# Kernel optimization log

Hardware: AMD Instinct MI355X
Metric: run time of the kernel (lower is better)

Reference implementation:

```python
import jax, jax.numpy as jnp
import numpy as np
import math

HEAD_DIM = 128
N_HEADS = 32
HIDDEN = 4096
ROPE_THETA = 10000.0
NEG = -100000.0


def _rope_cos_sin(pos):
    # pos: [B, L] int -> cos, sin: [B, L, HEAD_DIM]
    inv_freq = 1.0 / (ROPE_THETA ** (jnp.arange(0, HEAD_DIM, 2, dtype=jnp.float32) / HEAD_DIM))
    freqs = pos.astype(jnp.float32)[..., None] * inv_freq  # [B, L, HEAD_DIM//2]
    emb = jnp.concatenate([freqs, freqs], axis=-1)
    return jnp.cos(emb), jnp.sin(emb)


def _rotate_half(x):
    x1, x2 = x[..., : HEAD_DIM // 2], x[..., HEAD_DIM // 2 :]
    return jnp.concatenate([-x2, x1], axis=-1)


def _apply_rope(h, cos, sin):
    # h: [B, H, L, D], cos/sin: [B, L, D] -> unsqueeze head dim
    return h * cos[:, None] + _rotate_half(h) * sin[:, None]


def setup_inputs() -> dict:
    key = jax.random.key(0)
    ks = jax.random.split(key, 8)
    B, Q, K = 2, 1024, 2048
    inp = {
        "hidden_states": jax.random.normal(ks[0], (B, Q, HIDDEN), jnp.float32),
        "key_value_states": jax.random.normal(ks[1], (B, K, HIDDEN), jnp.float32),
        "Wq": jax.random.normal(ks[2], (HIDDEN, HIDDEN), jnp.float32) * 0.02,
        "Wk": jax.random.normal(ks[3], (HIDDEN, HIDDEN), jnp.float32) * 0.02,
        "Wv": jax.random.normal(ks[4], (HIDDEN, HIDDEN), jnp.float32) * 0.02,
        "Wo": jax.random.normal(ks[5], (HIDDEN, HIDDEN), jnp.float32) * 0.02,
        "position_ids": jnp.arange(B * Q, dtype=jnp.int32).reshape(B, Q),
        "text_position_ids": jnp.arange(B * K, dtype=jnp.int32).reshape(B, K),
        "simul_mask_idx": jnp.sort(jax.random.randint(ks[6], (B, Q), 0, K, jnp.int32), axis=-1),
        "window_size": jax.random.randint(ks[7], (B, Q), 0, 512, jnp.int32),
    }
    return inp


def reference(hidden_states, key_value_states, Wq, Wk, Wv, Wo,
              position_ids, text_position_ids, simul_mask_idx, window_size):
    B, Qlen, _ = hidden_states.shape
    Klen = key_value_states.shape[1]

    q = jnp.einsum('bqh,hd->bqd', hidden_states, Wq.T).reshape(B, Qlen, N_HEADS, HEAD_DIM).transpose(0, 2, 1, 3)
    k = jnp.einsum('bkh,hd->bkd', key_value_states, Wk.T).reshape(B, Klen, N_HEADS, HEAD_DIM).transpose(0, 2, 1, 3)
    v = jnp.einsum('bkh,hd->bkd', key_value_states, Wv.T).reshape(B, Klen, N_HEADS, HEAD_DIM).transpose(0, 2, 1, 3)

    cos, sin = _rope_cos_sin(position_ids)
    q = _apply_rope(q, cos, sin)
    t_cos, t_sin = _rope_cos_sin(text_position_ids)
    k = _apply_rope(k, t_cos, t_sin)

    scores = jnp.einsum('bhqd,bhkd->bhqk', q, k) / math.sqrt(HEAD_DIM)

    # simul windowed mask: key j visible for query i iff clamp(idx-w,0) <= j < idx
    idx = simul_mask_idx[:, None, :, None]          # [B,1,Q,1]
    w = window_size[:, None, :, None]               # [B,1,Q,1]
    tmp = jnp.arange(Klen, dtype=jnp.int32)         # [K]
    mask = (jnp.clip(idx - w, 0) <= tmp) & (tmp < idx)  # [B,1,Q,K]
    scores = jnp.where(mask, scores, NEG)

    probs = jax.nn.softmax(scores.astype(jnp.float32), axis=-1).astype(q.dtype)
    attn = jnp.einsum('bhqk,bhkd->bhqd', probs, v)
    attn = attn.transpose(0, 2, 1, 3).reshape(B, Qlen, HIDDEN)
    out = jnp.einsum('bqh,hd->bqd', attn, Wo.T)
    return out
```

## Files before the change

kernel.cpp:

```cpp
#include <hip/hip_runtime.h>
#include <stdint.h>

#define BATCH 2
#define QLEN 1024
#define KLEN 2048
#define NH 32
#define HD 128
#define HID 4096

typedef short bf16x8 __attribute__((ext_vector_type(8)));
typedef float f32x4 __attribute__((ext_vector_type(4)));
typedef unsigned short u16;

typedef const __attribute__((address_space(1))) void gvoid;
typedef __attribute__((address_space(3))) void lvoid;

__device__ __forceinline__ u16 f2bf(float f) {
  union { float f; uint32_t u; } x; x.f = f;
  uint32_t r = x.u + 0x7fffu + ((x.u >> 16) & 1u);
  return (u16)(r >> 16);
}
__device__ __forceinline__ float bf2f(u16 h) {
  union { uint32_t u; float f; } x; x.u = ((uint32_t)h) << 16;
  return x.f;
}
__device__ __forceinline__ f32x4 mfma16(bf16x8 a, bf16x8 b, f32x4 c) {
  return __builtin_amdgcn_mfma_f32_16x16x32_bf16(a, b, c, 0, 0, 0);
}
__device__ __forceinline__ void glds16(const u16* src, char* dst) {
  __builtin_amdgcn_global_load_lds((gvoid*)src, (lvoid*)dst, 16, 0, 0);
}

__global__ __launch_bounds__(256) void cvt_kernel(const float* __restrict__ in,
                                                  u16* __restrict__ out, int n) {
  int i = (blockIdx.x * 256 + threadIdx.x) * 8;
  if (i >= n) return;
  const float4* p = (const float4*)(in + i);
  float4 a = p[0], b = p[1];
  union { u16 h[8]; bf16x8 v; } u;
  u.h[0] = f2bf(a.x); u.h[1] = f2bf(a.y); u.h[2] = f2bf(a.z); u.h[3] = f2bf(a.w);
  u.h[4] = f2bf(b.x); u.h[5] = f2bf(b.y); u.h[6] = f2bf(b.z); u.h[7] = f2bf(b.w);
  *(bf16x8*)(out + i) = u.v;
}

#define RD_A(CB, ks, mf) (*(const bf16x8*)(lds + (CB) + (ks) * 16384 + (mf) * 1024 + rA))
#define RD_B(CB, ks, nf) (*(const bf16x8*)(lds + 65536 + (CB) + (ks) * 16384 + (nf) * 1024 + rB))

#define TILE256(CB, NB, K0N)                                                     \
  {                                                                              \
    bf16x8 af[4], bfr[4], af2[4];                                                \
    _Pragma("unroll") for (int x = 0; x < 4; x++) af[x] = RD_A(CB, 0, x);        \
    _Pragma("unroll") for (int x = 0; x < 4; x++) bfr[x] = RD_B(CB, 0, x);       \
    glds16(As0 + (K0N), dA + (NB));                                              \
    glds16(As1 + (K0N), dA + (NB) + 8192);                                       \
    __builtin_amdgcn_s_barrier();                                                \
    asm volatile("s_waitcnt lgkmcnt(0)" ::: "memory");                           \
    __builtin_amdgcn_sched_barrier(0);                                           \
    __builtin_amdgcn_s_setprio(1);                                               \
    _Pragma("unroll") for (int mf = 0; mf < 4; mf++)                             \
      _Pragma("unroll") for (int nf = 0; nf < 4; nf++)                           \
        acc[mf][nf] = mfma16(af[mf], bfr[nf], acc[mf][nf]);                      \
    __builtin_amdgcn_s_setprio(0);                                               \
    __builtin_amdgcn_s_barrier();                                                \
    _Pragma("unroll") for (int x = 0; x < 4; x++) af2[x] = RD_A(CB, 0, 4 + x);   \
    glds16(Bs0 + (K0N), dB + (NB));                                              \
    glds16(Bs1 + (K0N), dB + (NB) + 8192);                                       \
    asm volatile("s_waitcnt vmcnt(4)" ::: "memory");                             \
    __builtin_amdgcn_s_barrier();                                                \
    asm volatile("s_waitcnt lgkmcnt(0)" ::: "memory");                           \
    __builtin_amdgcn_sched_barrier(0);                                           \
    __builtin_amdgcn_s_setprio(1);                                               \
    _Pragma("unroll") for (int mf = 0; mf < 4; mf++)                             \
      _Pragma("unroll") for (int nf = 0; nf < 4; nf++)                           \
        acc[4 + mf][nf] = mfma16(af2[mf], bfr[nf], acc[4 + mf][nf]);             \
    __builtin_amdgcn_s_setprio(0);                                               \
    __builtin_amdgcn_s_barrier();                                                \
    _Pragma("unroll") for (int x = 0; x < 4; x++) af[x] = RD_A(CB, 1, x);        \
    _Pragma("unroll") for (int x = 0; x < 4; x++) bfr[x] = RD_B(CB, 1, x);       \
    glds16(As0 + (K0N) + 32, dA + (NB) + 16384);                                 \
    glds16(As1 + (K0N) + 32, dA + (NB) + 16384 + 8192);                          \
    __builtin_amdgcn_s_barrier();                                                \
    asm volatile("s_waitcnt lgkmcnt(0)" ::: "memory");                           \
    __builtin_amdgcn_sched_barrier(0);                                           \
    __builtin_amdgcn_s_setprio(1);                                               \
    _Pragma("unroll") for (int mf = 0; mf < 4; mf++)                             \
      _Pragma("unroll") for (int nf = 0; nf < 4; nf++)                           \
        acc[mf][nf] = mfma16(af[mf], bfr[nf], acc[mf][nf]);                      \
    __builtin_amdgcn_s_setprio(0);                                               \
    __builtin_amdgcn_s_barrier();                                                \
    _Pragma("unroll") for (int x = 0; x < 4; x++) af2[x] = RD_A(CB, 1, 4 + x);   \
    glds16(Bs0 + (K0N) + 32, dB + (NB) + 16384);                                 \
    glds16(Bs1 + (K0N) + 32, dB + (NB) + 16384 + 8192);                          \
    asm volatile("s_waitcnt vmcnt(4)" ::: "memory");                             \
    __builtin_amdgcn_s_barrier();                                                \
    asm volatile("s_waitcnt lgkmcnt(0)" ::: "memory");                           \
    __builtin_amdgcn_sched_barrier(0);                                           \
    __builtin_amdgcn_s_setprio(1);                                               \
    _Pragma("unroll") for (int mf = 0; mf < 4; mf++)                             \
      _Pragma("unroll") for (int nf = 0; nf < 4; nf++)                           \
        acc[4 + mf][nf] = mfma16(af2[mf], bfr[nf], acc[4 + mf][nf]);             \
    __builtin_amdgcn_s_setprio(0);                                               \
    __builtin_amdgcn_s_barrier();                                                \
  }

template <int EPI>
__global__ __launch_bounds__(512, 2) void gemm256(const u16* __restrict__ A,
                                                  const u16* __restrict__ Bw,
                                                  void* __restrict__ Cout,
                                                  int M, int N, int K) {
  (void)M;
  __shared__ alignas(16) char lds[131072];
  const int tid = threadIdx.x;
  const int lane = tid & 63, wv = tid >> 6;
  const int wvm = wv >> 2, wvn = wv & 3;
  const int g = lane >> 4, l16 = lane & 15;
  const int m0 = blockIdx.y * 256, n0 = blockIdx.x * 256;

  const int srow = tid >> 2;
  const int sg = (tid & 3) ^ ((srow >> 1) & 3);
  const u16* As0 = A + (size_t)(m0 + srow) * K + sg * 8;
  const u16* As1 = A + (size_t)(m0 + 128 + srow) * K + sg * 8;
  const u16* Bs0 = Bw + (size_t)(n0 + srow) * K + sg * 8;
  const u16* Bs1 = Bw + (size_t)(n0 + 128 + srow) * K + sg * 8;
  char* dA = lds + tid * 16;
  char* dB = lds + 65536 + tid * 16;

  const int rsw = (g ^ ((l16 >> 1) & 3)) << 4;
  const int rA = (wvm * 128 + l16) * 64 + rsw;
  const int rB = (wvn * 64 + l16) * 64 + rsw;

  f32x4 acc[8][4];
#pragma unroll
  for (int mf = 0; mf < 8; mf++)
#pragma unroll
    for (int nf = 0; nf < 4; nf++) acc[mf][nf] = (f32x4){0.f, 0.f, 0.f, 0.f};

  glds16(As0, dA);
  glds16(As1, dA + 8192);
  glds16(Bs0, dB);
  glds16(Bs1, dB + 8192);
  glds16(As0 + 32, dA + 16384);
  glds16(As1 + 32, dA + 16384 + 8192);
  glds16(Bs0 + 32, dB + 16384);
  glds16(Bs1 + 32, dB + 16384 + 8192);
  asm volatile("s_waitcnt vmcnt(4)" ::: "memory");
  __builtin_amdgcn_s_barrier();

  const int NT = K >> 6;
  for (int t = 0; t < NT; t += 2) {
    const int kA = (t + 1) * 64;
    TILE256(0, 32768, kA)
    const int kB = (((t + 2) < NT) ? (t + 2) : 0) * 64;
    TILE256(32768, 0, kB)
  }

  if (EPI == 2) {
    u16* C = (u16*)Cout;
#pragma unroll
    for (int mf = 0; mf < 8; mf++) {
      int rowb = m0 + wvm * 128 + mf * 16 + g * 4;
#pragma unroll
      for (int nf = 0; nf < 4; nf++) {
        int col = n0 + wvn * 64 + nf * 16 + l16;
#pragma unroll
        for (int j = 0; j < 4; j++)
          C[(size_t)(rowb + j) * N + col] = f2bf(acc[mf][nf][j]);
      }
    }
  } else {
    u16* C = (u16*)Cout;
#pragma unroll
    for (int mf = 0; mf < 8; mf++) {
      int rowb = m0 + wvm * 128 + mf * 16 + g * 4;
      int bb = rowb >> 11, tt = rowb & 2047;
#pragma unroll
      for (int nf = 0; nf < 4; nf++) {
        int col = n0 + wvn * 64 + nf * 16 + l16;
        uint64_t pk = (uint64_t)f2bf(acc[mf][nf][0]) |
                      ((uint64_t)f2bf(acc[mf][nf][1]) << 16) |
                      ((uint64_t)f2bf(acc[mf][nf][2]) << 32) |
                      ((uint64_t)f2bf(acc[mf][nf][3]) << 48);
        *(uint64_t*)(C + ((size_t)(bb * 4096 + col)) * 2048 + tt) = pk;
      }
    }
  }
}

#define RD_AT(CB, ks, mf) (*(const bf16x8*)(lds + (CB) + (ks) * 16384 + (mf) * 1024 + rA))
#define RD_BT(CB, ks, nf) (*(const bf16x8*)(lds + 65536 + (CB) + (ks) * 8192 + (nf) * 1024 + rB))

#define TILE256T(CB, CBB, NB, NBB, K0N)                                          \
  {                                                                              \
    bf16x8 af[4], bfr[4];                                                        \
    _Pragma("unroll") for (int x = 0; x < 4; x++) af[x] = RD_AT(CB, 0, x);       \
    _Pragma("unroll") for (int x = 0; x < 4; x++) bfr[x] = RD_BT(CBB, 0, x);     \
    glds16(AsT0 + (K0N), dAT + (NB));                                            \
    glds16(AsT1 + (K0N), dAT + (NB) + 8192);                                     \
    glds16(BsT0 + (K0N), dBT + (NBB));                                           \
    asm volatile("s_waitcnt vmcnt(3)" ::: "memory");                             \
    __builtin_amdgcn_s_barrier();                                                \
    asm volatile("s_waitcnt lgkmcnt(0)" ::: "memory");                           \
    __builtin_amdgcn_sched_barrier(0);                                           \
    __builtin_amdgcn_s_setprio(1);                                               \
    _Pragma("unroll") for (int mf = 0; mf < 4; mf++)                             \
      _Pragma("unroll") for (int nf = 0; nf < 4; nf++)                           \
        acc[mf][nf] = mfma16(af[mf], bfr[nf], acc[mf][nf]);                      \
    __builtin_amdgcn_s_setprio(0);                                               \
    __builtin_amdgcn_s_barrier();                                                \
    _Pragma("unroll") for (int x = 0; x < 4; x++) af[x] = RD_AT(CB, 1, x);       \
    _Pragma("unroll") for (int x = 0; x < 4; x++) bfr[x] = RD_BT(CBB, 1, x);     \
    glds16(AsT0 + (K0N) + 32, dAT + (NB) + 16384);                               \
    glds16(AsT1 + (K0N) + 32, dAT + (NB) + 16384 + 8192);                        \
    glds16(BsT0 + (K0N) + 32, dBT + (NBB) + 8192);                               \
    asm volatile("s_waitcnt vmcnt(3)" ::: "memory");                             \
    __builtin_amdgcn_s_barrier();                                                \
    asm volatile("s_waitcnt lgkmcnt(0)" ::: "memory");                           \
    __builtin_amdgcn_sched_barrier(0);                                           \
    __builtin_amdgcn_s_setprio(1);                                               \
    _Pragma("unroll") for (int mf = 0; mf < 4; mf++)                             \
      _Pragma("unroll") for (int nf = 0; nf < 4; nf++)                           \
        acc[mf][nf] = mfma16(af[mf], bfr[nf], acc[mf][nf]);                      \
    __builtin_amdgcn_s_setprio(0);                                               \
    __builtin_amdgcn_s_barrier();                                                \
  }

template <int EPI>
__global__ __launch_bounds__(512, 2) void gemm256T(const u16* __restrict__ W,
                                                   const u16* __restrict__ Act,
                                                   void* __restrict__ Cout,
                                                   int K) {
  __shared__ alignas(16) char lds[98304];
  const int tid = threadIdx.x;
  const int lane = tid & 63, wv = tid >> 6;
  const int wvm = wv >> 1, wvn = wv & 1;
  const int g = lane >> 4, l16 = lane & 15;
  const int m0 = blockIdx.y * 256;
  const int n0 = blockIdx.x * 128;

  const int srow = tid >> 2;
  const int sg = (tid & 3) ^ ((srow >> 1) & 3);
  const u16* AsT0 = W + (size_t)(m0 + srow) * K + sg * 8;
  const u16* AsT1 = W + (size_t)(m0 + 128 + srow) * K + sg * 8;
  const u16* BsT0 = Act + (size_t)(n0 + srow) * K + sg * 8;
  char* dAT = lds + tid * 16;
  char* dBT = lds + 65536 + tid * 16;

  const int rsw = (g ^ ((l16 >> 1) & 3)) << 4;
  const int rA = (wvm * 64 + l16) * 64 + rsw;
  const int rB = (wvn * 64 + l16) * 64 + rsw;

  f32x4 acc[4][4];
#pragma unroll
  for (int mf = 0; mf < 4; mf++)
#pragma unroll
    for (int nf = 0; nf < 4; nf++) acc[mf][nf] = (f32x4){0.f, 0.f, 0.f, 0.f};

  glds16(AsT0, dAT);
  glds16(AsT1, dAT + 8192);
  glds16(BsT0, dBT);
  glds16(AsT0 + 32, dAT + 16384);
  glds16(AsT1 + 32, dAT + 16384 + 8192);
  glds16(BsT0 + 32, dBT + 8192);
  asm volatile("s_waitcnt vmcnt(3)" ::: "memory");
  __builtin_amdgcn_s_barrier();

  const int NT = K >> 6;
  for (int t = 0; t < NT; t += 2) {
    const int kA = (t + 1) * 64;
    TILE256T(0, 0, 32768, 16384, kA)
    const int kB = (((t + 2) < NT) ? (t + 2) : 0) * 64;
    TILE256T(32768, 16384, 0, 0, kB)
  }

  if (EPI == 0) {
    float* C = (float*)Cout;
#pragma unroll
    for (int mf = 0; mf < 4; mf++) {
      int frow = m0 + wvm * 64 + mf * 16 + g * 4;
#pragma unroll
      for (int nf = 0; nf < 4; nf++) {
        int col = n0 + wvn * 64 + nf * 16 + l16;
        float4 v = {acc[mf][nf][0], acc[mf][nf][1], acc[mf][nf][2], acc[mf][nf][3]};
        *(float4*)(C + (size_t)col * HID + frow) = v;
      }
    }
  } else {
    u16* C = (u16*)Cout;
#pragma unroll
    for (int mf = 0; mf < 4; mf++) {
      int frow = m0 + wvm * 64 + mf * 16 + g * 4;
#pragma unroll
      for (int nf = 0; nf < 4; nf++) {
        int col = n0 + wvn * 64 + nf * 16 + l16;
        uint64_t pk = (uint64_t)f2bf(acc[mf][nf][0]) |
                      ((uint64_t)f2bf(acc[mf][nf][1]) << 16) |
                      ((uint64_t)f2bf(acc[mf][nf][2]) << 32) |
                      ((uint64_t)f2bf(acc[mf][nf][3]) << 48);
        *(uint64_t*)(C + (size_t)col * HID + frow) = pk;
      }
    }
  }
}

__global__ __launch_bounds__(256) void rope_kernel(const u16* __restrict__ x,
                                                   const int* __restrict__ pos,
                                                   u16* __restrict__ out,
                                                   int rowsPerB) {
  int row = blockIdx.x;
  int b = row / rowsPerB, r = row - b * rowsPerB;
  float p = (float)pos[row];
  int t = threadIdx.x;
  int h = t >> 3, i0 = (t & 7) * 8;
  const u16* xr = x + (size_t)row * HID + h * HD;
  bf16x8 lov = *(const bf16x8*)(xr + i0);
  bf16x8 hiv = *(const bf16x8*)(xr + 64 + i0);
  union { u16 h[8]; bf16x8 v; } olo, ohi;
#pragma unroll
  for (int j = 0; j < 8; j++) {
    float lo = bf2f((u16)lov[j]);
    float hi = bf2f((u16)hiv[j]);
    float f = exp2f(-(float)(i0 + j) * (13.287712379549449f / 64.0f));
    float ang = p * f;
    float s, c;
    sincosf(ang, &s, &c);
    olo.h[j] = f2bf(lo * c - hi * s);
    ohi.h[j] = f2bf(hi * c + lo * s);
  }
  u16* ob = out + ((size_t)((b * NH + h) * rowsPerB) + r) * HD;
  *(bf16x8*)(ob + i0) = olo.v;
  *(bf16x8*)(ob + 64 + i0) = ohi.v;
}

__global__ __launch_bounds__(256) void vmean_kernel(const u16* __restrict__ vt,
                                                    float* __restrict__ vm) {
  int row = blockIdx.x * 4 + (threadIdx.x >> 6);
  int lane = threadIdx.x & 63;
  const u16* p = vt + (size_t)row * KLEN;
  float s = 0.f;
#pragma unroll
  for (int it = 0; it < 4; it++) {
    bf16x8 v = *(const bf16x8*)(p + it * 512 + lane * 8);
#pragma unroll
    for (int j = 0; j < 8; j++) s += bf2f((u16)v[j]);
  }
  for (int off = 32; off; off >>= 1) s += __shfl_xor(s, off);
  if (lane == 0) vm[row] = s * (1.0f / (float)KLEN);
}

__global__ __launch_bounds__(256, 2) void attn_kernel(
    const u16* __restrict__ qb, const u16* __restrict__ kb,
    const u16* __restrict__ vt, const float* __restrict__ vm,
    const int* __restrict__ idxA, const int* __restrict__ wA,
    u16* __restrict__ aout) {
  __shared__ u16 Ks[32][136];
  __shared__ u16 Vs[128][40];
  __shared__ u16 Ps[4][16][40];
  __shared__ int sS[64], sE[64], sRange[2];

  const int tid = threadIdx.x, lane = tid & 63, wv = tid >> 6;
  const int g = lane >> 4, l16 = lane & 15;
  const int blk = blockIdx.x;
  const int qt = blk & 15, bh = blk >> 4, b = bh >> 5, h = bh & 31;
  const int q0 = qt * 64;
  const float SCALE = 0.08838834764831845f;

  if (tid < 64) {
    int e = idxA[b * QLEN + q0 + tid];
    int w = wA[b * QLEN + q0 + tid];
    int s = e - w;
    if (s < 0) s = 0;
    sS[tid] = s;
    sE[tid] = e;
  }
  __syncthreads();
  if (wv == 0) {
    int s_ = sS[lane], e_ = sE[lane];
    int mn = (e_ > s_) ? s_ : 0x7fffffff;
    int mx = (e_ > s_) ? e_ : 0;
    for (int off = 32; off; off >>= 1) {
      mn = min(mn, __shfl_xor(mn, off));
      mx = max(mx, __shfl_xor(mx, off));
    }
    if (lane == 0) { sRange[0] = mn; sRange[1] = mx; }
  }
  __syncthreads();
  const int klo = sRange[0], khi = sRange[1];

  int rs[4], re[4];
#pragma unroll
  for (int r = 0; r < 4; r++) {
    rs[r] = sS[wv * 16 + g * 4 + r];
    re[r] = sE[wv * 16 + g * 4 + r];
  }

  bf16x8 qf[4];
  {
    const u16* qp = qb + ((size_t)(bh * QLEN + q0 + wv * 16 + l16)) * HD + g * 8;
#pragma unroll
    for (int s4 = 0; s4 < 4; s4++) qf[s4] = *(const bf16x8*)(qp + s4 * 32);
  }

  f32x4 acc[8];
#pragma unroll
  for (int db = 0; db < 8; db++) acc[db] = (f32x4){0.f, 0.f, 0.f, 0.f};
  float mrow[4] = {-1e30f, -1e30f, -1e30f, -1e30f};
  float lsum[4] = {0.f, 0.f, 0.f, 0.f};

  if (klo < khi) {
    for (int t0 = (klo & ~31); t0 < khi; t0 += 32) {
      {
        int idx = tid * 8;
        int kr = idx >> 7, kc = idx & 127;
        *(bf16x8*)(&Ks[kr][kc]) =
            *(const bf16x8*)(kb + ((size_t)(bh * KLEN + t0 + kr)) * HD + kc);
        int kr2 = kr + 16;
        *(bf16x8*)(&Ks[kr2][kc]) =
            *(const bf16x8*)(kb + ((size_t)(bh * KLEN + t0 + kr2)) * HD + kc);
        int vr = idx >> 5, vc = idx & 31;
        *(bf16x8*)(&Vs[vr][vc]) =
            *(const bf16x8*)(vt + ((size_t)(bh * HD + vr)) * KLEN + t0 + vc);
        int vr2 = vr + 64;
        *(bf16x8*)(&Vs[vr2][vc]) =
            *(const bf16x8*)(vt + ((size_t)(bh * HD + vr2)) * KLEN + t0 + vc);
      }
      __syncthreads();

      f32x4 sc0 = (f32x4){0.f, 0.f, 0.f, 0.f};
      f32x4 sc1 = (f32x4){0.f, 0.f, 0.f, 0.f};
#pragma unroll
      for (int s4 = 0; s4 < 4; s4++) {
        bf16x8 k0 = *(const bf16x8*)(&Ks[l16][s4 * 32 + g * 8]);
        bf16x8 k1 = *(const bf16x8*)(&Ks[16 + l16][s4 * 32 + g * 8]);
        sc0 = mfma16(qf[s4], k0, sc0);
        sc1 = mfma16(qf[s4], k1, sc1);
      }

      float resc[4];
#pragma unroll
      for (int r = 0; r < 4; r++) {
        float v0 = sc0[r] * SCALE, v1 = sc1[r] * SCALE;
        int t_0 = t0 + l16, t_1 = t0 + 16 + l16;
        v0 = (t_0 >= rs[r] && t_0 < re[r]) ? v0 : -1e30f;
        v1 = (t_1 >= rs[r] && t_1 < re[r]) ? v1 : -1e30f;
        float mx = fmaxf(v0, v1);
        mx = fmaxf(mx, __shfl_xor(mx, 1));
        mx = fmaxf(mx, __shfl_xor(mx, 2));
        mx = fmaxf(mx, __shfl_xor(mx, 4));
        mx = fmaxf(mx, __shfl_xor(mx, 8));
        float mn = fmaxf(mrow[r], mx);
        float rc = __expf(mrow[r] - mn);
        float p0 = __expf(v0 - mn), p1 = __expf(v1 - mn);
        mrow[r] = mn;
        resc[r] = rc;
        float ps = p0 + p1;
        ps += __shfl_xor(ps, 1);
        ps += __shfl_xor(ps, 2);
        ps += __shfl_xor(ps, 4);
        ps += __shfl_xor(ps, 8);
        lsum[r] = lsum[r] * rc + ps;
        Ps[wv][g * 4 + r][l16] = f2bf(p0);
        Ps[wv][g * 4 + r][16 + l16] = f2bf(p1);
      }
#pragma unroll
      for (int db = 0; db < 8; db++) {
#pragma unroll
        for (int r = 0; r < 4; r++) acc[db][r] *= resc[r];
      }
      bf16x8 pf = *(const bf16x8*)(&Ps[wv][l16][g * 8]);
#pragma unroll
      for (int db = 0; db < 8; db++) {
        bf16x8 vf = *(const bf16x8*)(&Vs[db * 16 + l16][g * 8]);
        acc[db] = mfma16(pf, vf, acc[db]);
      }
      __syncthreads();
    }
  }

#pragma unroll
  for (int r = 0; r < 4; r++) {
    int lr = wv * 16 + g * 4 + r;
    int q = q0 + lr;
    bool empty = (re[r] <= rs[r]);
    float inv = empty ? 0.f : 1.0f / lsum[r];
    u16* orow = aout + ((size_t)(b * QLEN + q)) * HID + h * HD;
#pragma unroll
    for (int db = 0; db < 8; db++) {
      float o = empty ? vm[bh * HD + db * 16 + l16] : acc[db][r] * inv;
      orow[db * 16 + l16] = f2bf(o);
    }
  }
}

extern "C" void kernel_launch(void* const* d_in, const int* in_sizes, int n_in,
                              void* d_out, int out_size, void* d_ws, size_t ws_size,
                              hipStream_t stream) {
  (void)in_sizes; (void)n_in; (void)out_size; (void)ws_size;
  const float* hs = (const float*)d_in[0];
  const float* kvs = (const float*)d_in[1];
  const float* Wq = (const float*)d_in[2];
  const float* Wk = (const float*)d_in[3];
  const float* Wv = (const float*)d_in[4];
  const float* Wo = (const float*)d_in[5];
  const int* pos = (const int*)d_in[6];
  const int* tpos = (const int*)d_in[7];
  const int* sidx = (const int*)d_in[8];
  const int* wsz = (const int*)d_in[9];
  float* out = (float*)d_out;

  char* ws = (char*)d_ws;
  size_t off = 0;
  auto alloc = [&](size_t bytes) -> void* {
    void* p = ws + off;
    off += (bytes + 255) & ~(size_t)255;
    return p;
  };
  const size_t WN = (size_t)HID * HID;
  const size_t NQ = (size_t)BATCH * QLEN * HID;
  const size_t NK = (size_t)BATCH * KLEN * HID;

  u16* wbuf = (u16*)alloc(WN * 2);
  u16* hid_b = (u16*)alloc(NQ * 2);
  u16* kv_b = (u16*)alloc(NK * 2);
  u16* sc_b = (u16*)alloc(NK * 2);
  u16* q_b = (u16*)alloc(NQ * 2);
  u16* k_b = (u16*)alloc(NK * 2);
  u16* vt_b = (u16*)alloc(NK * 2);
  float* vmean = (float*)alloc((size_t)BATCH * NH * HD * 4);

  cvt_kernel<<<(int)(NQ / 2048), 256, 0, stream>>>(hs, hid_b, (int)NQ);
  cvt_kernel<<<(int)(NK / 2048), 256, 0, stream>>>(kvs, kv_b, (int)NK);

  cvt_kernel<<<(int)(WN / 2048), 256, 0, stream>>>(Wq, wbuf, (int)WN);
  gemm256T<2><<<dim3(BATCH * QLEN / 128, HID / 256), 512, 0, stream>>>(
      wbuf, hid_b, sc_b, HID);
  rope_kernel<<<BATCH * QLEN, 256, 0, stream>>>(sc_b, pos, q_b, QLEN);

  cvt_kernel<<<(int)(WN / 2048), 256, 0, stream>>>(Wk, wbuf, (int)WN);
  gemm256<2><<<dim3(HID / 256, BATCH * KLEN / 256), 512, 0, stream>>>(
      kv_b, wbuf, sc_b, BATCH * KLEN, HID, HID);
  rope_kernel<<<BATCH * KLEN, 256, 0, stream>>>(sc_b, tpos, k_b, KLEN);

  cvt_kernel<<<(int)(WN / 2048), 256, 0, stream>>>(Wv, wbuf, (int)WN);
  gemm256<1><<<dim3(HID / 256, BATCH * KLEN / 256), 512, 0, stream>>>(
      kv_b, wbuf, vt_b, BATCH * KLEN, HID, HID);
  vmean_kernel<<<BATCH * NH * HD / 4, 256, 0, stream>>>(vt_b, vmean);

  attn_kernel<<<BATCH * NH * (QLEN / 64), 256, 0, stream>>>(
      q_b, k_b, vt_b, vmean, sidx, wsz, sc_b);

  cvt_kernel<<<(int)(WN / 2048), 256, 0, stream>>>(Wo, wbuf, (int)WN);
  gemm256T<0><<<dim3(BATCH * QLEN / 128, HID / 256), 512, 0, stream>>>(
      wbuf, sc_b, out, HID);
}
```

Baseline: 589.6 us.

## Deepen GEMM prefetch pipeline to triple-buffered LDS and reorder staging loads

The transposed GEMM (used for the Q and O projections) moves from double to triple buffering in LDS, growing shared memory to 144KB. It prefetches two K-tiles ahead and drains the last tile in a separate epilogue, with K hardcoded to HID. In the 256x256 GEMM, the A and B staging loads are reordered so that both halves are issued earlier, with wait counts adjusted to match. The aim is to hide global-load latency behind MFMA work. The cost is higher LDS use, which may prevent two blocks per CU despite launch_bounds(512,2).

```diff
diff --git a/kernel.cpp b/kernel.cpp
--- a/kernel.cpp
+++ b/kernel.cpp
@@ -53,6 +53,8 @@
     _Pragma("unroll") for (int x = 0; x < 4; x++) bfr[x] = RD_B(CB, 0, x);       \
     glds16(As0 + (K0N), dA + (NB));                                              \
     glds16(As1 + (K0N), dA + (NB) + 8192);                                       \
+    glds16(Bs0 + (K0N), dB + (NB));                                              \
+    glds16(Bs1 + (K0N), dB + (NB) + 8192);                                       \
     __builtin_amdgcn_s_barrier();                                                \
     asm volatile("s_waitcnt lgkmcnt(0)" ::: "memory");                           \
     __builtin_amdgcn_sched_barrier(0);                                           \
@@ -63,9 +65,9 @@
     __builtin_amdgcn_s_setprio(0);                                               \
     __builtin_amdgcn_s_barrier();                                                \
     _Pragma("unroll") for (int x = 0; x < 4; x++) af2[x] = RD_A(CB, 0, 4 + x);   \
-    glds16(Bs0 + (K0N), dB + (NB));                                              \
-    glds16(Bs1 + (K0N), dB + (NB) + 8192);                                       \
-    asm volatile("s_waitcnt vmcnt(4)" ::: "memory");                             \
+    glds16(As0 + (K0N) + 32, dA + (NB) + 16384);                                 \
+    glds16(As1 + (K0N) + 32, dA + (NB) + 16384 + 8192);                          \
+    asm volatile("s_waitcnt vmcnt(6)" ::: "memory");                             \
     __builtin_amdgcn_s_barrier();                                                \
     asm volatile("s_waitcnt lgkmcnt(0)" ::: "memory");                           \
     __builtin_amdgcn_sched_barrier(0);                                           \
@@ -77,8 +79,8 @@
     __builtin_amdgcn_s_barrier();                                                \
     _Pragma("unroll") for (int x = 0; x < 4; x++) af[x] = RD_A(CB, 1, x);        \
     _Pragma("unroll") for (int x = 0; x < 4; x++) bfr[x] = RD_B(CB, 1, x);       \
-    glds16(As0 + (K0N) + 32, dA + (NB) + 16384);                                 \
-    glds16(As1 + (K0N) + 32, dA + (NB) + 16384 + 8192);                          \
+    glds16(Bs0 + (K0N) + 32, dB + (NB) + 16384);                                 \
+    glds16(Bs1 + (K0N) + 32, dB + (NB) + 16384 + 8192);                          \
     __builtin_amdgcn_s_barrier();                                                \
     asm volatile("s_waitcnt lgkmcnt(0)" ::: "memory");                           \
     __builtin_amdgcn_sched_barrier(0);                                           \
@@ -89,8 +91,6 @@
     __builtin_amdgcn_s_setprio(0);                                               \
     __builtin_amdgcn_s_barrier();                                                \
     _Pragma("unroll") for (int x = 0; x < 4; x++) af2[x] = RD_A(CB, 1, 4 + x);   \
-    glds16(Bs0 + (K0N) + 32, dB + (NB) + 16384);                                 \
-    glds16(Bs1 + (K0N) + 32, dB + (NB) + 16384 + 8192);                          \
     asm volatile("s_waitcnt vmcnt(4)" ::: "memory");                             \
     __builtin_amdgcn_s_barrier();                                                \
     asm volatile("s_waitcnt lgkmcnt(0)" ::: "memory");                           \
@@ -186,18 +186,27 @@
   }
 }
 
-#define RD_AT(CB, ks, mf) (*(const bf16x8*)(lds + (CB) + (ks) * 16384 + (mf) * 1024 + rA))
-#define RD_BT(CB, ks, nf) (*(const bf16x8*)(lds + 65536 + (CB) + (ks) * 8192 + (nf) * 1024 + rB))
-
-#define TILE256T(CB, CBB, NB, NBB, K0N)                                          \
+#define RD_AT(BUF, ks, mf) \
+  (*(const bf16x8*)(lds + (BUF) * 32768 + (ks) * 16384 + (mf) * 1024 + rA))
+#define RD_BT(BUF, ks, nf) \
+  (*(const bf16x8*)(lds + 98304 + (BUF) * 16384 + (ks) * 8192 + (nf) * 1024 + rB))
+
+#define STG_H0(BUF, K0N)                                    \
+  glds16(AsT0 + (K0N), dAT + (BUF) * 32768);                \
+  glds16(AsT1 + (K0N), dAT + (BUF) * 32768 + 8192);         \
+  glds16(BsT0 + (K0N), dBT + (BUF) * 16384);
+
+#define STG_H1(BUF, K0N)                                    \
+  glds16(AsT0 + (K0N) + 32, dAT + (BUF) * 32768 + 16384);   \
+  glds16(AsT1 + (K0N) + 32, dAT + (BUF) * 32768 + 16384 + 8192); \
+  glds16(BsT0 + (K0N) + 32, dBT + (BUF) * 16384 + 8192);
+
+#define TILE256T(CUR, STG, K0N)                                                  \
   {                                                                              \
     bf16x8 af[4], bfr[4];                                                        \
-    _Pragma("unroll") for (int x = 0; x < 4; x++) af[x] = RD_AT(CB, 0, x);       \
-    _Pragma("unroll") for (int x = 0; x < 4; x++) bfr[x] = RD_BT(CBB, 0, x);     \
-    glds16(AsT0 + (K0N), dAT + (NB));                                            \
-    glds16(AsT1 + (K0N), dAT + (NB) + 8192);                                     \
-    glds16(BsT0 + (K0N), dBT + (NBB));                                           \
-    asm volatile("s_waitcnt vmcnt(3)" ::: "memory");                             \
+    _Pragma("unroll") for (int x = 0; x < 4; x++) af[x] = RD_AT(CUR, 0, x);      \
+    _Pragma("unroll") for (int x = 0; x < 4; x++) bfr[x] = RD_BT(CUR, 0, x);     \
+    STG_H0(STG, K0N)                                                             \
     __builtin_amdgcn_s_barrier();                                                \
     asm volatile("s_waitcnt lgkmcnt(0)" ::: "memory");                           \
     __builtin_amdgcn_sched_barrier(0);                                           \
@@ -207,12 +216,10 @@
         acc[mf][nf] = mfma16(af[mf], bfr[nf], acc[mf][nf]);                      \
     __builtin_amdgcn_s_setprio(0);                                               \
     __builtin_amdgcn_s_barrier();                                                \
-    _Pragma("unroll") for (int x = 0; x < 4; x++) af[x] = RD_AT(CB, 1, x);       \
-    _Pragma("unroll") for (int x = 0; x < 4; x++) bfr[x] = RD_BT(CBB, 1, x);     \
-    glds16(AsT0 + (K0N) + 32, dAT + (NB) + 16384);                               \
-    glds16(AsT1 + (K0N) + 32, dAT + (NB) + 16384 + 8192);                        \
-    glds16(BsT0 + (K0N) + 32, dBT + (NBB) + 8192);                               \
-    asm volatile("s_waitcnt vmcnt(3)" ::: "memory");                             \
+    _Pragma("unroll") for (int x = 0; x < 4; x++) af[x] = RD_AT(CUR, 1, x);      \
+    _Pragma("unroll") for (int x = 0; x < 4; x++) bfr[x] = RD_BT(CUR, 1, x);     \
+    STG_H1(STG, K0N)                                                             \
+    asm volatile("s_waitcnt vmcnt(6)" ::: "memory");                             \
     __builtin_amdgcn_s_barrier();                                                \
     asm volatile("s_waitcnt lgkmcnt(0)" ::: "memory");                           \
     __builtin_amdgcn_sched_barrier(0);                                           \
@@ -227,9 +234,9 @@
 template <int EPI>
 __global__ __launch_bounds__(512, 2) void gemm256T(const u16* __restrict__ W,
                                                    const u16* __restrict__ Act,
-                                                   void* __restrict__ Cout,
-                                                   int K) {
-  __shared__ alignas(16) char lds[98304];
+                                                   void* __restrict__ Cout) {
+  const int K = HID;
+  __shared__ alignas(16) char lds[147456];
   const int tid = threadIdx.x;
   const int lane = tid & 63, wv = tid >> 6;
   const int wvm = wv >> 1, wvn = wv & 1;
@@ -243,7 +250,7 @@
   const u16* AsT1 = W + (size_t)(m0 + 128 + srow) * K + sg * 8;
   const u16* BsT0 = Act + (size_t)(n0 + srow) * K + sg * 8;
   char* dAT = lds + tid * 16;
-  char* dBT = lds + 65536 + tid * 16;
+  char* dBT = lds + 98304 + tid * 16;
 
   const int rsw = (g ^ ((l16 >> 1) & 3)) << 4;
   const int rA = (wvm * 64 + l16) * 64 + rsw;
@@ -255,21 +262,41 @@
 #pragma unroll
     for (int nf = 0; nf < 4; nf++) acc[mf][nf] = (f32x4){0.f, 0.f, 0.f, 0.f};
 
-  glds16(AsT0, dAT);
-  glds16(AsT1, dAT + 8192);
-  glds16(BsT0, dBT);
-  glds16(AsT0 + 32, dAT + 16384);
-  glds16(AsT1 + 32, dAT + 16384 + 8192);
-  glds16(BsT0 + 32, dBT + 8192);
-  asm volatile("s_waitcnt vmcnt(3)" ::: "memory");
+  STG_H0(0, 0)
+  STG_H1(0, 0)
+  STG_H0(1, 64)
+  STG_H1(1, 64)
+  asm volatile("s_waitcnt vmcnt(6)" ::: "memory");
   __builtin_amdgcn_s_barrier();
 
-  const int NT = K >> 6;
-  for (int t = 0; t < NT; t += 2) {
-    const int kA = (t + 1) * 64;
-    TILE256T(0, 0, 32768, 16384, kA)
-    const int kB = (((t + 2) < NT) ? (t + 2) : 0) * 64;
-    TILE256T(32768, 16384, 0, 0, kB)
+  for (int t = 0; t < 63; t += 3) {
+    const int k1 = (t + 2) * 64;
+    const int k2 = (t + 3) * 64;
+    const int k3 = ((t + 4) < 64) ? (t + 4) * 64 : 0;
+    TILE256T(0, 2, k1)
+    TILE256T(1, 0, k2)
+    TILE256T(2, 1, k3)
+  }
+  {
+    bf16x8 af[4], bfr[4];
+#pragma unroll
+    for (int x = 0; x < 4; x++) af[x] = RD_AT(0, 0, x);
+#pragma unroll
+    for (int x = 0; x < 4; x++) bfr[x] = RD_BT(0, 0, x);
+#pragma unroll
+    for (int mf = 0; mf < 4; mf++)
+#pragma unroll
+      for (int nf = 0; nf < 4; nf++)
+        acc[mf][nf] = mfma16(af[mf], bfr[nf], acc[mf][nf]);
+#pragma unroll
+    for (int x = 0; x < 4; x++) af[x] = RD_AT(0, 1, x);
+#pragma unroll
+    for (int x = 0; x < 4; x++) bfr[x] = RD_BT(0, 1, x);
+#pragma unroll
+    for (int mf = 0; mf < 4; mf++)
+#pragma unroll
+      for (int nf = 0; nf < 4; nf++)
+        acc[mf][nf] = mfma16(af[mf], bfr[nf], acc[mf][nf]);
   }
 
   if (EPI == 0) {
@@ -532,7 +559,7 @@
 
   cvt_kernel<<<(int)(WN / 2048), 256, 0, stream>>>(Wq, wbuf, (int)WN);
   gemm256T<2><<<dim3(BATCH * QLEN / 128, HID / 256), 512, 0, stream>>>(
-      wbuf, hid_b, sc_b, HID);
+      wbuf, hid_b, sc_b);
   rope_kernel<<<BATCH * QLEN, 256, 0, stream>>>(sc_b, pos, q_b, QLEN);
 
   cvt_kernel<<<(int)(WN / 2048), 256, 0, stream>>>(Wk, wbuf, (int)WN);
@@ -550,5 +577,5 @@
 
   cvt_kernel<<<(int)(WN / 2048), 256, 0, stream>>>(Wo, wbuf, (int)WN);
   gemm256T<0><<<dim3(BATCH * QLEN / 128, HID / 256), 512, 0, stream>>>(
-      wbuf, sc_b, out, HID);
-}
+      wbuf, sc_b, out);
+}
```

Result: no change. 586.1 us (-0.6%).
